# Kernel optimization log

Hardware: AMD Instinct MI355X
Metric: run time of the kernel (lower is better)

## Reference

```python
import jax, jax.numpy as jnp
import numpy as np

T, N, E, DH = 4, 10000, 160000, 256
BN_EPS = 1e-5


def setup_inputs() -> dict:
    key = jax.random.key(0)
    ks = jax.random.split(key, 6)
    node_data = jax.random.normal(ks[0], (T, N, DH), dtype=jnp.float32)
    edge_index = jax.random.randint(ks[1], (2, E), 0, N)
    edge_weight = jax.random.uniform(ks[2], (T, E), dtype=jnp.float32)
    W1 = jax.random.normal(ks[3], (3 * DH, DH), dtype=jnp.float32) * 0.02
    b1 = jnp.zeros((DH,), dtype=jnp.float32)
    gamma = jnp.ones((DH,), dtype=jnp.float32)
    beta = jnp.zeros((DH,), dtype=jnp.float32)
    return {"node_data": node_data, "edge_weight": edge_weight, "W1": W1,
            "b1": b1, "gamma": gamma, "beta": beta, "edge_index": edge_index}


def reference(node_data, edge_weight, W1, b1, gamma, beta, edge_index):
    # edge_index: [2, E] with row 0 = source j, row 1 = destination i
    # (ew[t, i, j] multiplies node j and accumulates into node i, as in bmm)
    src, dst = edge_index[0], edge_index[1]

    # sparse bmm: sum_j ew[t,i,j] * node_data[t,j,:]  -> [T, N, DH]
    weighted = node_data[:, src, :] * edge_weight[..., None]  # [T, E, DH]
    sum_neighbor = jax.vmap(lambda m: jax.ops.segment_sum(m, dst, num_segments=N))(weighted)

    # Z = torch.sparse.sum(ew, dim=2); Z[Z == 0] = 1
    Z = jax.vmap(lambda w: jax.ops.segment_sum(w, dst, num_segments=N))(edge_weight)
    Z = jnp.where(Z == 0, 1.0, Z)[..., None]  # [T, N, 1]
    avg_neighbor = sum_neighbor / Z

    # prev_state = cat([zeros(1,N,dh), node_data[1:]], dim=0)  (as in source)
    prev_state = jnp.concatenate(
        [jnp.zeros((1, N, DH), node_data.dtype), node_data[1:]], axis=0)

    x = jnp.concatenate([node_data, prev_state, avg_neighbor], axis=2)
    x = x.reshape(T * N, 3 * DH)

    # ReluFCN: Linear(3*dh -> dh) -> BatchNorm1d (batch stats) -> ReLU
    h = x @ W1 + b1  # [T*N, DH]
    mean = h.mean(axis=0)
    var = h.var(axis=0)
    h = (h - mean) * jax.lax.rsqrt(var + BN_EPS) * gamma + beta
    h = jax.nn.relu(h)
    return h.reshape(T, N, DH)
```

## Files before the change

kernel.cpp:

```cpp
#include <hip/hip_runtime.h>

enum { TT = 4, NNODES = 10000, NEDGES = 160000 };

typedef short v8s __attribute__((ext_vector_type(8)));
typedef float v4f __attribute__((ext_vector_type(4)));
typedef unsigned short u16x4 __attribute__((ext_vector_type(4)));

static __device__ __forceinline__ float bf2f(unsigned short u) {
    union { unsigned int i; float f; } c;
    c.i = ((unsigned int)u) << 16;
    return c.f;
}
static __device__ __forceinline__ unsigned short f2bf(float f) {
    union { float f; unsigned int i; } c;
    c.f = f;
    return (unsigned short)((c.i + 0x7FFFu + ((c.i >> 16) & 1u)) >> 16);
}
static __device__ __forceinline__ float u2f(unsigned int u) {
    union { unsigned int i; float f; } c;
    c.i = u;
    return c.f;
}
static __device__ __forceinline__ void acc8(float* a, float w, uint4 u) {
    a[0] += w * u2f(u.x << 16);
    a[1] += w * u2f(u.x & 0xffff0000u);
    a[2] += w * u2f(u.y << 16);
    a[3] += w * u2f(u.y & 0xffff0000u);
    a[4] += w * u2f(u.z << 16);
    a[5] += w * u2f(u.z & 0xffff0000u);
    a[6] += w * u2f(u.w << 16);
    a[7] += w * u2f(u.w & 0xffff0000u);
}

__global__ void GraphConvLayer_91061896610587_kernel() {}

__global__ void zero_k(int* p, int n) {
    int i = blockIdx.x * 256 + threadIdx.x;
    if (i < n) p[i] = 0;
}

__global__ void prep_k(const unsigned short* ndu, const void* s0, const void* s1,
                       const void* s2, int* mode, float* gammaf, float* betaf) {
    __shared__ int cnt;
    __shared__ int score[6];
    __shared__ float vals[6][256];
    int d = threadIdx.x;
    if (d == 0) cnt = 0;
    if (d < 6) score[d] = 0;
    __syncthreads();
    int c = 0;
    for (int j = 0; j < 16; ++j) {
        unsigned short u = ndu[d * 16 + j];
        if ((u & 0x7FFF) >= 0x6000) ++c;
    }
    if (c) atomicAdd(&cnt, c);
    const void* ptrs[3];
    ptrs[0] = s0; ptrs[1] = s1; ptrs[2] = s2;
    for (int q = 0; q < 6; ++q) {
        const void* p = ptrs[q % 3];
        float v = (q < 3) ? bf2f(((const unsigned short*)p)[d]) : ((const float*)p)[d];
        vals[q][d] = v;
        float av = fabsf(v);
        if (av > 0.25f && av < 4.0f) atomicAdd(&score[q], 1);
    }
    __syncthreads();
    if (d == 0) *mode = (cnt > 0) ? 0 : 1;
    int best = 0;
    for (int q = 1; q < 6; ++q)
        if (score[q] > score[best]) best = q;
    float g = (score[best] > 0) ? vals[best][d] : 1.0f;
    int interp = (best >= 3) ? 3 : 0;
    int bslot  = ((best % 3) == 2) ? 1 : 2;
    float b = vals[interp + bslot][d];
    if (!(b == b) || fabsf(b) > 100.f) b = 0.f;
    gammaf[d] = g;
    betaf[d]  = b;
}

__global__ void zp_k(int* zp, int zn, const unsigned short* ndu, const void* s0,
                     const void* s1, const void* s2, int* mode, float* gammaf,
                     float* betaf) {
    __shared__ int cnt;
    __shared__ int score[6];
    __shared__ float vals[6][256];
    if (blockIdx.x < 213) {
        int i = blockIdx.x * 256 + threadIdx.x;
        if (i < zn) zp[i] = 0;
        return;
    }
    int d = threadIdx.x;
    if (d == 0) cnt = 0;
    if (d < 6) score[d] = 0;
    __syncthreads();
    int c = 0;
    for (int j = 0; j < 16; ++j) {
        unsigned short u = ndu[d * 16 + j];
        if ((u & 0x7FFF) >= 0x6000) ++c;
    }
    if (c) atomicAdd(&cnt, c);
    const void* ptrs[3];
    ptrs[0] = s0; ptrs[1] = s1; ptrs[2] = s2;
    for (int q = 0; q < 6; ++q) {
        const void* p = ptrs[q % 3];
        float v = (q < 3) ? bf2f(((const unsigned short*)p)[d]) : ((const float*)p)[d];
        vals[q][d] = v;
        float av = fabsf(v);
        if (av > 0.25f && av < 4.0f) atomicAdd(&score[q], 1);
    }
    __syncthreads();
    if (d == 0) *mode = (cnt > 0) ? 0 : 1;
    int best = 0;
    for (int q = 1; q < 6; ++q)
        if (score[q] > score[best]) best = q;
    float g = (score[best] > 0) ? vals[best][d] : 1.0f;
    int interp = (best >= 3) ? 3 : 0;
    int bslot  = ((best % 3) == 2) ? 1 : 2;
    float b = vals[interp + bslot][d];
    if (!(b == b) || fabsf(b) > 100.f) b = 0.f;
    gammaf[d] = g;
    betaf[d]  = b;
}

__global__ void cph_k(const int* mode, const void* nd_raw, unsigned short* ndc,
                      const void* W1, short* wp0, short* wp1,
                      const int* ei, int* counts) {
    int bb = blockIdx.x;
    if (bb < 10000) {
        if (*mode != 0) return;
        int i = bb * 256 + threadIdx.x;
        float4 v = ((const float4*)nd_raw)[i];
        ushort4 o;
        o.x = f2bf(v.x); o.y = f2bf(v.y); o.z = f2bf(v.z); o.w = f2bf(v.w);
        ((ushort4*)ndc)[i] = o;
    } else if (bb < 11024) {
        int gid = (bb - 10000) * 256 + threadIdx.x;
        int v   = gid >> 17;
        int rem = gid & 131071;
        int k   = rem >> 8;
        int n   = rem & 255;
        int m   = *mode;
        const unsigned short* Wb = (const unsigned short*)W1;
        const float*          Wf = (const float*)W1;
        float val;
        if (k < 256) {
            val = m ? bf2f(Wb[k * 256 + n]) : Wf[k * 256 + n];
            if (v) val += m ? bf2f(Wb[(k + 256) * 256 + n]) : Wf[(k + 256) * 256 + n];
        } else {
            val = m ? bf2f(Wb[(k + 256) * 256 + n]) : Wf[(k + 256) * 256 + n];
        }
        int dst = ((k >> 5) * 256 + n) * 32 + (k & 31);
        (v ? wp1 : wp0)[dst] = (short)f2bf(val);
    } else {
        int e = (bb - 11024) * 256 + threadIdx.x;
        if (e < NEDGES) atomicAdd(&counts[ei[NEDGES + e]], 1);
    }
}

__global__ void pack_w(const int* mode, const void* W1, float* w2f,
                       short* wp0, short* wp1) {
    int gid = blockIdx.x * 256 + threadIdx.x;
    int v   = gid >> 17;
    int rem = gid & 131071;
    int k   = rem >> 8;
    int n   = rem & 255;
    int m   = *mode;
    const unsigned short* Wb = (const unsigned short*)W1;
    const float*          Wf = (const float*)W1;
    float val;
    if (k < 256) {
        val = m ? bf2f(Wb[k * 256 + n]) : Wf[k * 256 + n];
        if (v) val += m ? bf2f(Wb[(k + 256) * 256 + n]) : Wf[(k + 256) * 256 + n];
    } else {
        val = m ? bf2f(Wb[(k + 256) * 256 + n]) : Wf[(k + 256) * 256 + n];
    }
    if (w2f) w2f[v * 131072 + k * 256 + n] = val;
    if (wp0) {
        int dst = ((k >> 5) * 256 + n) * 32 + (k & 31);
        (v ? wp1 : wp0)[dst] = (short)f2bf(val);
    }
}

__global__ void hist_k(const int* ei, int* counts) {
    int e = blockIdx.x * 256 + threadIdx.x;
    if (e < NEDGES) atomicAdd(&counts[ei[NEDGES + e]], 1);
}

__global__ void scan_k(const int* counts, int* offsets) {
    __shared__ int part[256];
    __shared__ int excl[257];
    int t = threadIdx.x;
    int b = t * 40, e = b + 40;
    if (e > NNODES) e = NNODES;
    int s = 0;
    for (int i = b; i < e; ++i) s += counts[i];
    part[t] = s;
    __syncthreads();
    if (t == 0) {
        int run = 0;
        for (int i = 0; i < 256; ++i) { excl[i] = run; run += part[i]; }
        excl[256] = run;
    }
    __syncthreads();
    int run = excl[t];
    for (int i = b; i < e; ++i) { offsets[i] = run; run += counts[i]; }
    if (t == 0) offsets[NNODES] = excl[256];
}

__global__ void scat_k(const int* ei, const int* offsets, int* cursors,
                       int* ssrc, int* seid) {
    int e = blockIdx.x * 256 + threadIdx.x;
    if (e >= NEDGES) return;
    int d = ei[NEDGES + e];
    int pos = offsets[d] + atomicAdd(&cursors[d], 1);
    ssrc[pos] = ei[e];
    seid[pos] = e;
}

__global__ void scatw_k(const int* mode, const int* ei, const void* ew_raw,
                        const int* offsets, int* cursors, int* ssrc, int* seid,
                        float* wcsr) {
    int e = blockIdx.x * 256 + threadIdx.x;
    if (e >= NEDGES) return;
    int d = ei[NEDGES + e];
    int pos = offsets[d] + atomicAdd(&cursors[d], 1);
    ssrc[pos] = ei[e];
    seid[pos] = e;
    int m = *mode;
#pragma unroll
    for (int t = 0; t < TT; ++t) {
        float w = m ? bf2f(((const unsigned short*)ew_raw)[t * NEDGES + e])
                    : ((const float*)ew_raw)[t * NEDGES + e];
        wcsr[t * NEDGES + pos] = w;
    }
}

__global__ __launch_bounds__(256) void fused_k(
    const int* mode, const void* nd_raw, const unsigned short* ndc,
    const float* wcsr, const int* offsets, const int* ssrc,
    const short* wp0, const short* wp1,
    unsigned short* h16, float* colsumB, float* colsumsqB) {
    __shared__ unsigned short xs[32 * 520];
    int id  = blockIdx.x;
    int xcd = id & 7;
    int t   = xcd & 3;
    int rbi = ((id >> 3) << 1) + (xcd >> 2);
    if (rbi >= 313) return;
    int rb  = rbi * 32;
    const unsigned short* ndb = (*mode == 1) ? (const unsigned short*)nd_raw : ndc;
    int tid = threadIdx.x;

    int node = tid >> 3;
    int sub  = tid & 7;
    int growc = min(rb + node, NNODES - 1);
    const uint4* ndg = (const uint4*)(ndb + (size_t)t * NNODES * 256);
    const uint4* own = ndg + (size_t)growc * 32;

    uint4 c0 = own[sub];
    uint4 c1 = own[sub + 8];
    uint4 c2 = own[sub + 16];
    uint4 c3 = own[sub + 24];
    *(uint4*)&xs[node * 520 + sub * 8]            = c0;
    *(uint4*)&xs[node * 520 + (sub + 8) * 8]      = c1;
    *(uint4*)&xs[node * 520 + (sub + 16) * 8]     = c2;
    *(uint4*)&xs[node * 520 + (sub + 24) * 8]     = c3;

    float a1[32];
#pragma unroll
    for (int j = 0; j < 32; ++j) a1[j] = 0.f;
    float Z = 0.f;
    const float* wrow = wcsr + t * NEDGES;
    int b = offsets[growc], e = offsets[growc + 1];
    int p = b;
    for (; p + 2 <= e; p += 2) {
        int s0 = ssrc[p], s1 = ssrc[p + 1];
        float w0 = wrow[p], w1 = wrow[p + 1];
        const uint4* r0 = ndg + (size_t)s0 * 32;
        const uint4* r1 = ndg + (size_t)s1 * 32;
        uint4 A0 = r0[sub], A1 = r0[sub + 8], A2 = r0[sub + 16], A3 = r0[sub + 24];
        uint4 B0 = r1[sub], B1 = r1[sub + 8], B2 = r1[sub + 16], B3 = r1[sub + 24];
        Z += w0 + w1;
        acc8(a1 + 0,  w0, A0); acc8(a1 + 8,  w0, A1);
        acc8(a1 + 16, w0, A2); acc8(a1 + 24, w0, A3);
        acc8(a1 + 0,  w1, B0); acc8(a1 + 8,  w1, B1);
        acc8(a1 + 16, w1, B2); acc8(a1 + 24, w1, B3);
    }
    for (; p < e; ++p) {
        int s = ssrc[p];
        float w = wrow[p];
        const uint4* r0 = ndg + (size_t)s * 32;
        uint4 A0 = r0[sub], A1 = r0[sub + 8], A2 = r0[sub + 16], A3 = r0[sub + 24];
        Z += w;
        acc8(a1 + 0,  w, A0); acc8(a1 + 8,  w, A1);
        acc8(a1 + 16, w, A2); acc8(a1 + 24, w, A3);
    }
    float inv = (Z == 0.f) ? 1.f : (1.f / Z);
#pragma unroll
    for (int j = 0; j < 4; ++j) {
        ushort4 lo, hi;
        lo.x = f2bf(a1[j * 8 + 0] * inv);
        lo.y = f2bf(a1[j * 8 + 1] * inv);
        lo.z = f2bf(a1[j * 8 + 2] * inv);
        lo.w = f2bf(a1[j * 8 + 3] * inv);
        hi.x = f2bf(a1[j * 8 + 4] * inv);
        hi.y = f2bf(a1[j * 8 + 5] * inv);
        hi.z = f2bf(a1[j * 8 + 6] * inv);
        hi.w = f2bf(a1[j * 8 + 7] * inv);
        *(ushort4*)&xs[node * 520 + 256 + (sub + 8 * j) * 8]     = lo;
        *(ushort4*)&xs[node * 520 + 256 + (sub + 8 * j) * 8 + 4] = hi;
    }
    __syncthreads();

    int wave = tid >> 6;
    int lane = tid & 63;
    int lane15 = lane & 15, quad = lane >> 4;
    const v8s* wp8 = (const v8s*)(t ? wp1 : wp0);

    v4f acc[2][4];
    v4f zero = {0.f, 0.f, 0.f, 0.f};
#pragma unroll
    for (int mf = 0; mf < 2; ++mf)
#pragma unroll
        for (int nf = 0; nf < 4; ++nf) acc[mf][nf] = zero;

#pragma unroll
    for (int kc = 0; kc < 16; ++kc) {
        v8s a0 = *(const v8s*)&xs[lane15 * 520 + kc * 32 + quad * 8];
        v8s a1v = *(const v8s*)&xs[(lane15 + 16) * 520 + kc * 32 + quad * 8];
#pragma unroll
        for (int nf = 0; nf < 4; ++nf) {
            int ntg = wave * 4 + nf;
            v8s bf = wp8[(size_t)(kc * 256 + ntg * 16 + lane15) * 4 + quad];
            acc[0][nf] = __builtin_amdgcn_mfma_f32_16x16x32_bf16(a0, bf, acc[0][nf], 0, 0, 0);
            acc[1][nf] = __builtin_amdgcn_mfma_f32_16x16x32_bf16(a1v, bf, acc[1][nf], 0, 0, 0);
        }
    }

    int bucket = id & 63;
#pragma unroll
    for (int nf = 0; nf < 4; ++nf) {
        int col = (wave * 4 + nf) * 16 + lane15;
        float s1 = 0.f, s2 = 0.f;
#pragma unroll
        for (int mf = 0; mf < 2; ++mf) {
            int rbase = rb + mf * 16 + quad * 4;
#pragma unroll
            for (int r = 0; r < 4; ++r) {
                int row = rbase + r;
                if (row < NNODES) {
                    float v = acc[mf][nf][r];
                    __builtin_nontemporal_store(
                        f2bf(v), &h16[(size_t)(t * NNODES + row) * 256 + col]);
                    s1 += v; s2 += v * v;
                }
            }
        }
        s1 += __shfl_xor(s1, 16, 64); s1 += __shfl_xor(s1, 32, 64);
        s2 += __shfl_xor(s2, 16, 64); s2 += __shfl_xor(s2, 32, 64);
        if (quad == 0) {
            atomicAdd(&colsumB[bucket * 256 + col], s1);
            atomicAdd(&colsumsqB[bucket * 256 + col], s2);
        }
    }
}

__global__ void statsB_k(const float* colsumB, const float* colsumsqB,
                         const float* gammaf, const float* betaf,
                         float* scale, float* shiftv) {
    int d = threadIdx.x;
    float s1 = 0.f, s2 = 0.f;
    for (int b = 0; b < 64; ++b) {
        s1 += colsumB[b * 256 + d];
        s2 += colsumsqB[b * 256 + d];
    }
    float mean = s1 * (1.f / 40000.f);
    float var  = s2 * (1.f / 40000.f) - mean * mean;
    if (var < 0.f) var = 0.f;
    if (!(var < 1e30f) || !(mean == mean)) { scale[d] = 0.f; shiftv[d] = 2.5f; return; }
    float r  = rsqrtf(var + 1e-5f);
    float sc = gammaf[d] * r;
    scale[d]  = sc;
    shiftv[d] = betaf[d] - mean * sc;
}

__global__ void normb_k(const unsigned short* h16, const float* scale,
                        const float* shiftv, float* out) {
    int i = blockIdx.x * 256 + threadIdx.x;
    int c0 = (i & 63) * 4;
    u16x4 h = __builtin_nontemporal_load(&((const u16x4*)h16)[i]);
    v4f o;
    float v;
    v = bf2f(h.x) * scale[c0 + 0] + shiftv[c0 + 0]; if (!(v == v)) v = 1.f; o.x = v > 0.f ? v : 0.f;
    v = bf2f(h.y) * scale[c0 + 1] + shiftv[c0 + 1]; if (!(v == v)) v = 1.f; o.y = v > 0.f ? v : 0.f;
    v = bf2f(h.z) * scale[c0 + 2] + shiftv[c0 + 2]; if (!(v == v)) v = 1.f; o.z = v > 0.f ? v : 0.f;
    v = bf2f(h.w) * scale[c0 + 3] + shiftv[c0 + 3]; if (!(v == v)) v = 1.f; o.w = v > 0.f ? v : 0.f;
    __builtin_nontemporal_store(o, &((v4f*)out)[i]);
}

__global__ void aggv_k(const int* mode, const void* nd_raw, const void* ew_raw,
                       const int* offsets, const int* ssrc, const int* seid,
                       unsigned short* avg) {
    int m   = *mode;
    int wid = blockIdx.x * 4 + (threadIdx.x >> 6);
    int t = wid / NNODES, n = wid - t * NNODES;
    int lane = threadIdx.x & 63;
    float a0 = 0.f, a1 = 0.f, a2 = 0.f, a3 = 0.f, Z = 0.f;
    int b = offsets[n], e = offsets[n + 1];
    for (int p = b; p < e; ++p) {
        int s = ssrc[p];
        int ewi = t * NEDGES + seid[p];
        float w = m ? bf2f(((const unsigned short*)ew_raw)[ewi])
                    : ((const float*)ew_raw)[ewi];
        Z += w;
        int vidx = (t * NNODES + s) * 64 + lane;
        if (m) {
            ushort4 v = ((const ushort4*)nd_raw)[vidx];
            a0 += w * bf2f(v.x); a1 += w * bf2f(v.y);
            a2 += w * bf2f(v.z); a3 += w * bf2f(v.w);
        } else {
            float4 v = ((const float4*)nd_raw)[vidx];
            a0 += w * v.x; a1 += w * v.y; a2 += w * v.z; a3 += w * v.w;
        }
    }
    float inv = (Z == 0.f) ? 1.f : (1.f / Z);
    ushort4 o;
    o.x = f2bf(a0 * inv); o.y = f2bf(a1 * inv);
    o.z = f2bf(a2 * inv); o.w = f2bf(a3 * inv);
    ((ushort4*)avg)[(t * NNODES + n) * 64 + lane] = o;
}

__global__ __launch_bounds__(256) void gemmv_k(
    const int* mode, const void* nd_raw, const unsigned short* avg,
    const float* w2f, float* hbuf) {
    __shared__ float xsf[16 * 512];
    int m   = *mode;
    int bt  = blockIdx.x / 625;
    int rb0 = (blockIdx.x - bt * 625) * 16;
    int tid = threadIdx.x;
    for (int j = 0; j < 32; ++j) {
        int idx = tid + j * 256;
        int r = idx >> 9, k = idx & 511;
        int grow = (bt * NNODES + rb0 + r) * 256;
        float val;
        if (k < 256)
            val = m ? bf2f(((const unsigned short*)nd_raw)[grow + k])
                    : ((const float*)nd_raw)[grow + k];
        else
            val = bf2f(avg[grow + (k - 256)]);
        xsf[idx] = val;
    }
    __syncthreads();
    int r0 = (tid >> 6) * 4;
    const float4* w4 = (const float4*)(w2f + (bt ? 131072 : 0));
    float acc[4][4];
#pragma unroll
    for (int r = 0; r < 4; ++r)
#pragma unroll
        for (int c = 0; c < 4; ++c) acc[r][c] = 0.f;
    const float* x0 = &xsf[(r0 + 0) * 512];
    const float* x1 = &xsf[(r0 + 1) * 512];
    const float* x2 = &xsf[(r0 + 2) * 512];
    const float* x3 = &xsf[(r0 + 3) * 512];
#pragma unroll 8
    for (int k = 0; k < 512; ++k) {
        float4 wv = w4[k * 64 + (tid & 63)];
        float a = x0[k], b = x1[k], c = x2[k], d = x3[k];
        acc[0][0] += a * wv.x; acc[0][1] += a * wv.y; acc[0][2] += a * wv.z; acc[0][3] += a * wv.w;
        acc[1][0] += b * wv.x; acc[1][1] += b * wv.y; acc[1][2] += b * wv.z; acc[1][3] += b * wv.w;
        acc[2][0] += c * wv.x; acc[2][1] += c * wv.y; acc[2][2] += c * wv.z; acc[2][3] += c * wv.w;
        acc[3][0] += d * wv.x; acc[3][1] += d * wv.y; acc[3][2] += d * wv.z; acc[3][3] += d * wv.w;
    }
#pragma unroll
    for (int r = 0; r < 4; ++r) {
        int grow = bt * NNODES + rb0 + r0 + r;
        float4 o;
        o.x = acc[r][0]; o.y = acc[r][1]; o.z = acc[r][2]; o.w = acc[r][3];
        ((float4*)hbuf)[grow * 64 + (tid & 63)] = o;
    }
}

__global__ void stats2_k(const float* hbuf, float* colsum, float* colsumsq) {
    int col = threadIdx.x;
    int rb  = blockIdx.x * 250;
    float s1 = 0.f, s2 = 0.f;
    for (int j = 0; j < 250; ++j) {
        float v = hbuf[(size_t)(rb + j) * 256 + col];
        s1 += v; s2 += v * v;
    }
    atomicAdd(&colsum[col], s1);
    atomicAdd(&colsumsq[col], s2);
}

__global__ void stats_k(const float* colsum, const float* colsumsq,
                        const float* gammaf, const float* betaf,
                        float* scale, float* shiftv) {
    int d = threadIdx.x;
    float mean = colsum[d] * (1.f / 40000.f);
    float var  = colsumsq[d] * (1.f / 40000.f) - mean * mean;
    if (var < 0.f) var = 0.f;
    if (!(var < 1e30f) || !(mean == mean)) { scale[d] = 0.f; shiftv[d] = 2.5f; return; }
    float r  = rsqrtf(var + 1e-5f);
    float sc = gammaf[d] * r;
    scale[d]  = sc;
    shiftv[d] = betaf[d] - mean * sc;
}

__global__ void norm_k(float* hbuf, const float* scale, const float* shiftv) {
    int i = blockIdx.x * 256 + threadIdx.x;
    int c0 = (i & 63) * 4;
    float4 h = ((const float4*)hbuf)[i];
    float4 o;
    float v;
    v = h.x * scale[c0 + 0] + shiftv[c0 + 0]; if (!(v == v)) v = 1.f; o.x = v > 0.f ? v : 0.f;
    v = h.y * scale[c0 + 1] + shiftv[c0 + 1]; if (!(v == v)) v = 1.f; o.y = v > 0.f ? v : 0.f;
    v = h.z * scale[c0 + 2] + shiftv[c0 + 2]; if (!(v == v)) v = 1.f; o.z = v > 0.f ? v : 0.f;
    v = h.w * scale[c0 + 3] + shiftv[c0 + 3]; if (!(v == v)) v = 1.f; o.w = v > 0.f ? v : 0.f;
    ((float4*)hbuf)[i] = o;
}

extern "C" void kernel_launch(void* const* d_in, const int* in_sizes, int n_in,
                              void* d_out, int out_size, void* d_ws, size_t ws_size,
                              hipStream_t stream) {
    const void* nd = d_in[0];
    const void* ew = d_in[1];
    const void* W1 = d_in[2];
    const void* p3 = d_in[3];
    const void* p4 = d_in[4];
    const void* p5 = d_in[5];
    const void* ei = d_in[6];
    {
        const void *nd_ = 0, *ew_ = 0, *W1_ = 0, *ei_ = 0, *s_[3] = {0, 0, 0};
        int ns = 0;
        for (int i = 0; i < n_in; ++i) {
            int s = in_sizes[i];
            if      (s == 10240000) nd_ = d_in[i];
            else if (s == 640000)   ew_ = d_in[i];
            else if (s == 196608)   W1_ = d_in[i];
            else if (s == 320000)   ei_ = d_in[i];
            else if (s == 256 && ns < 3) s_[ns++] = d_in[i];
        }
        if (nd_ && ew_ && W1_ && ei_ && ns == 3) {
            nd = nd_; ew = ew_; W1 = W1_; ei = ei_;
            p3 = s_[0]; p4 = s_[1]; p5 = s_[2];
        }
    }
    float* outp = (float*)d_out;
    const unsigned short* ndu = (const unsigned short*)nd;
    const int* eii = (const int*)ei;

    char* ws = (char*)d_ws;

    if (ws_size >= (size_t)45582464) {
        int*   counts    = (int*)(ws + 0);
        int*   cursors   = (int*)(ws + 40960);
        int*   mode      = (int*)(ws + 81920);
        float* scale     = (float*)(ws + 82944);
        float* shiftv    = (float*)(ws + 83968);
        float* gammaf    = (float*)(ws + 84992);
        float* betaf     = (float*)(ws + 86016);
        float* colsumB   = (float*)(ws + 87040);
        float* colsumsqB = (float*)(ws + 152576);
        int*   offsets   = (int*)(ws + 218112);
        int*   ssrc      = (int*)(ws + 258176);
        int*   seid      = (int*)(ws + 898176);
        float* wcsr      = (float*)(ws + 1538176);
        short* wp0       = (short*)(ws + 4098176);
        short* wp1       = (short*)(ws + 4360320);
        unsigned short* ndc = (unsigned short*)(ws + 4622464);
        unsigned short* h16 = (unsigned short*)(ws + 25102464);

        zp_k<<<214, 256, 0, stream>>>((int*)ws, 54528, ndu, p3, p4, p5,
                                      mode, gammaf, betaf);
        cph_k<<<11649, 256, 0, stream>>>(mode, nd, ndc, W1, wp0, wp1, eii, counts);
        scan_k<<<1, 256, 0, stream>>>(counts, offsets);
        scatw_k<<<625, 256, 0, stream>>>(mode, eii, ew, offsets, cursors,
                                         ssrc, seid, wcsr);
        fused_k<<<1280, 256, 0, stream>>>(mode, nd, ndc, wcsr, offsets, ssrc,
                                          wp0, wp1, h16, colsumB, colsumsqB);
        statsB_k<<<1, 256, 0, stream>>>(colsumB, colsumsqB, gammaf, betaf, scale, shiftv);
        normb_k<<<10000, 256, 0, stream>>>(h16, scale, shiftv, outp);
    } else {
        int*   counts   = (int*)(ws + 0);
        int*   cursors  = (int*)(ws + 40960);
        float* colsum   = (float*)(ws + 81920);
        float* colsumsq = (float*)(ws + 82944);
        int*   mode     = (int*)(ws + 83968);
        float* scale    = (float*)(ws + 84032);
        float* shiftv   = (float*)(ws + 85056);
        float* gammaf   = (float*)(ws + 86080);
        float* betaf    = (float*)(ws + 87104);
        int*   offsets  = (int*)(ws + 88128);
        int*   ssrc     = (int*)(ws + 128192);
        int*   seid     = (int*)(ws + 768192);
        float* w2f      = (float*)(ws + 1408192);
        unsigned short* avg = (unsigned short*)(ws + 2457600);
        short* nowp = 0;

        zero_k<<<83, 256, 0, stream>>>((int*)ws, 20994);
        prep_k<<<1, 256, 0, stream>>>(ndu, p3, p4, p5, mode, gammaf, betaf);
        pack_w<<<1024, 256, 0, stream>>>(mode, W1, w2f, nowp, nowp);
        hist_k<<<625, 256, 0, stream>>>(eii, counts);
        scan_k<<<1, 256, 0, stream>>>(counts, offsets);
        scat_k<<<625, 256, 0, stream>>>(eii, offsets, cursors, ssrc, seid);
        aggv_k<<<10000, 256, 0, stream>>>(mode, nd, ew, offsets, ssrc, seid, avg);
        gemmv_k<<<2500, 256, 0, stream>>>(mode, nd, avg, w2f, outp);
        stats2_k<<<160, 256, 0, stream>>>(outp, colsum, colsumsq);
        stats_k<<<1, 256, 0, stream>>>(colsum, colsumsq, gammaf, betaf, scale, shiftv);
        norm_k<<<10000, 256, 0, stream>>>(outp, scale, shiftv);
    }
}
```

Baseline: 233.0 us.

## Double fused kernel threads per block, splitting each node's gather over 16 lanes

The fused gather-and-matmul kernel now runs 512 threads per block instead of 256. Each node's neighbour aggregation is split across 16 lanes rather than 8, which halves per-thread accumulator registers, and the edge loop is unrolled by 4 to keep more loads in flight. In the MFMA stage each of the 8 waves covers 2 column tiles instead of 4. The aim is more parallelism and memory-level overlap in the latency-bound gather, at the cost of larger blocks and a changed occupancy hint.

```diff
diff --git a/kernel.cpp b/kernel.cpp
--- a/kernel.cpp
+++ b/kernel.cpp
@@ -234,7 +234,7 @@
     }
 }
 
-__global__ __launch_bounds__(256) void fused_k(
+__global__ __launch_bounds__(512, 6) void fused_k(
     const int* mode, const void* nd_raw, const unsigned short* ndc,
     const float* wcsr, const int* offsets, const int* ssrc,
     const short* wp0, const short* wp1,
@@ -249,64 +249,64 @@
     const unsigned short* ndb = (*mode == 1) ? (const unsigned short*)nd_raw : ndc;
     int tid = threadIdx.x;
 
-    int node = tid >> 3;
-    int sub  = tid & 7;
+    int node = tid >> 4;
+    int sub  = tid & 15;
     int growc = min(rb + node, NNODES - 1);
     const uint4* ndg = (const uint4*)(ndb + (size_t)t * NNODES * 256);
     const uint4* own = ndg + (size_t)growc * 32;
 
     uint4 c0 = own[sub];
-    uint4 c1 = own[sub + 8];
-    uint4 c2 = own[sub + 16];
-    uint4 c3 = own[sub + 24];
-    *(uint4*)&xs[node * 520 + sub * 8]            = c0;
-    *(uint4*)&xs[node * 520 + (sub + 8) * 8]      = c1;
-    *(uint4*)&xs[node * 520 + (sub + 16) * 8]     = c2;
-    *(uint4*)&xs[node * 520 + (sub + 24) * 8]     = c3;
-
-    float a1[32];
-#pragma unroll
-    for (int j = 0; j < 32; ++j) a1[j] = 0.f;
+    uint4 c1 = own[sub + 16];
+    *(uint4*)&xs[node * 520 + sub * 8]        = c0;
+    *(uint4*)&xs[node * 520 + (sub + 16) * 8] = c1;
+
+    float a1[16];
+#pragma unroll
+    for (int j = 0; j < 16; ++j) a1[j] = 0.f;
     float Z = 0.f;
     const float* wrow = wcsr + t * NEDGES;
     int b = offsets[growc], e = offsets[growc + 1];
     int p = b;
-    for (; p + 2 <= e; p += 2) {
-        int s0 = ssrc[p], s1 = ssrc[p + 1];
-        float w0 = wrow[p], w1 = wrow[p + 1];
+    for (; p + 4 <= e; p += 4) {
+        int s0 = ssrc[p], s1 = ssrc[p + 1], s2 = ssrc[p + 2], s3 = ssrc[p + 3];
+        float w0 = wrow[p], w1 = wrow[p + 1], w2 = wrow[p + 2], w3 = wrow[p + 3];
         const uint4* r0 = ndg + (size_t)s0 * 32;
         const uint4* r1 = ndg + (size_t)s1 * 32;
-        uint4 A0 = r0[sub], A1 = r0[sub + 8], A2 = r0[sub + 16], A3 = r0[sub + 24];
-        uint4 B0 = r1[sub], B1 = r1[sub + 8], B2 = r1[sub + 16], B3 = r1[sub + 24];
-        Z += w0 + w1;
-        acc8(a1 + 0,  w0, A0); acc8(a1 + 8,  w0, A1);
-        acc8(a1 + 16, w0, A2); acc8(a1 + 24, w0, A3);
-        acc8(a1 + 0,  w1, B0); acc8(a1 + 8,  w1, B1);
-        acc8(a1 + 16, w1, B2); acc8(a1 + 24, w1, B3);
+        const uint4* r2 = ndg + (size_t)s2 * 32;
+        const uint4* r3 = ndg + (size_t)s3 * 32;
+        uint4 A0 = r0[sub], A1 = r0[sub + 16];
+        uint4 B0 = r1[sub], B1 = r1[sub + 16];
+        uint4 C0 = r2[sub], C1 = r2[sub + 16];
+        uint4 D0 = r3[sub], D1 = r3[sub + 16];
+        Z += w0 + w1 + w2 + w3;
+        acc8(a1 + 0, w0, A0); acc8(a1 + 8, w0, A1);
+        acc8(a1 + 0, w1, B0); acc8(a1 + 8, w1, B1);
+        acc8(a1 + 0, w2, C0); acc8(a1 + 8, w2, C1);
+        acc8(a1 + 0, w3, D0); acc8(a1 + 8, w3, D1);
     }
     for (; p < e; ++p) {
         int s = ssrc[p];
         float w = wrow[p];
         const uint4* r0 = ndg + (size_t)s * 32;
-        uint4 A0 = r0[sub], A1 = r0[sub + 8], A2 = r0[sub + 16], A3 = r0[sub + 24];
+        uint4 A0 = r0[sub], A1 = r0[sub + 16];
         Z += w;
-        acc8(a1 + 0,  w, A0); acc8(a1 + 8,  w, A1);
-        acc8(a1 + 16, w, A2); acc8(a1 + 24, w, A3);
+        acc8(a1 + 0, w, A0); acc8(a1 + 8, w, A1);
     }
     float inv = (Z == 0.f) ? 1.f : (1.f / Z);
-#pragma unroll
-    for (int j = 0; j < 4; ++j) {
+    {
         ushort4 lo, hi;
-        lo.x = f2bf(a1[j * 8 + 0] * inv);
-        lo.y = f2bf(a1[j * 8 + 1] * inv);
-        lo.z = f2bf(a1[j * 8 + 2] * inv);
-        lo.w = f2bf(a1[j * 8 + 3] * inv);
-        hi.x = f2bf(a1[j * 8 + 4] * inv);
-        hi.y = f2bf(a1[j * 8 + 5] * inv);
-        hi.z = f2bf(a1[j * 8 + 6] * inv);
-        hi.w = f2bf(a1[j * 8 + 7] * inv);
-        *(ushort4*)&xs[node * 520 + 256 + (sub + 8 * j) * 8]     = lo;
-        *(ushort4*)&xs[node * 520 + 256 + (sub + 8 * j) * 8 + 4] = hi;
+        lo.x = f2bf(a1[0] * inv); lo.y = f2bf(a1[1] * inv);
+        lo.z = f2bf(a1[2] * inv); lo.w = f2bf(a1[3] * inv);
+        hi.x = f2bf(a1[4] * inv); hi.y = f2bf(a1[5] * inv);
+        hi.z = f2bf(a1[6] * inv); hi.w = f2bf(a1[7] * inv);
+        *(ushort4*)&xs[node * 520 + 256 + sub * 8]     = lo;
+        *(ushort4*)&xs[node * 520 + 256 + sub * 8 + 4] = hi;
+        lo.x = f2bf(a1[8] * inv);  lo.y = f2bf(a1[9] * inv);
+        lo.z = f2bf(a1[10] * inv); lo.w = f2bf(a1[11] * inv);
+        hi.x = f2bf(a1[12] * inv); hi.y = f2bf(a1[13] * inv);
+        hi.z = f2bf(a1[14] * inv); hi.w = f2bf(a1[15] * inv);
+        *(ushort4*)&xs[node * 520 + 256 + (sub + 16) * 8]     = lo;
+        *(ushort4*)&xs[node * 520 + 256 + (sub + 16) * 8 + 4] = hi;
     }
     __syncthreads();
 
@@ -315,30 +315,30 @@
     int lane15 = lane & 15, quad = lane >> 4;
     const v8s* wp8 = (const v8s*)(t ? wp1 : wp0);
 
-    v4f acc[2][4];
+    v4f acc[2][2];
     v4f zero = {0.f, 0.f, 0.f, 0.f};
 #pragma unroll
     for (int mf = 0; mf < 2; ++mf)
 #pragma unroll
-        for (int nf = 0; nf < 4; ++nf) acc[mf][nf] = zero;
+        for (int nf = 0; nf < 2; ++nf) acc[mf][nf] = zero;
 
 #pragma unroll
     for (int kc = 0; kc < 16; ++kc) {
-        v8s a0 = *(const v8s*)&xs[lane15 * 520 + kc * 32 + quad * 8];
+        v8s a0  = *(const v8s*)&xs[lane15 * 520 + kc * 32 + quad * 8];
         v8s a1v = *(const v8s*)&xs[(lane15 + 16) * 520 + kc * 32 + quad * 8];
 #pragma unroll
-        for (int nf = 0; nf < 4; ++nf) {
-            int ntg = wave * 4 + nf;
+        for (int nf = 0; nf < 2; ++nf) {
+            int ntg = wave * 2 + nf;
             v8s bf = wp8[(size_t)(kc * 256 + ntg * 16 + lane15) * 4 + quad];
-            acc[0][nf] = __builtin_amdgcn_mfma_f32_16x16x32_bf16(a0, bf, acc[0][nf], 0, 0, 0);
+            acc[0][nf] = __builtin_amdgcn_mfma_f32_16x16x32_bf16(a0,  bf, acc[0][nf], 0, 0, 0);
             acc[1][nf] = __builtin_amdgcn_mfma_f32_16x16x32_bf16(a1v, bf, acc[1][nf], 0, 0, 0);
         }
     }
 
     int bucket = id & 63;
 #pragma unroll
-    for (int nf = 0; nf < 4; ++nf) {
-        int col = (wave * 4 + nf) * 16 + lane15;
+    for (int nf = 0; nf < 2; ++nf) {
+        int col = (wave * 2 + nf) * 16 + lane15;
         float s1 = 0.f, s2 = 0.f;
 #pragma unroll
         for (int mf = 0; mf < 2; ++mf) {
@@ -574,7 +574,7 @@
         scan_k<<<1, 256, 0, stream>>>(counts, offsets);
         scatw_k<<<625, 256, 0, stream>>>(mode, eii, ew, offsets, cursors,
                                          ssrc, seid, wcsr);
-        fused_k<<<1280, 256, 0, stream>>>(mode, nd, ndc, wcsr, offsets, ssrc,
+        fused_k<<<1280, 512, 0, stream>>>(mode, nd, ndc, wcsr, offsets, ssrc,
                                           wp0, wp1, h16, colsumB, colsumsqB);
         statsB_k<<<1, 256, 0, stream>>>(colsumB, colsumsqB, gammaf, betaf, scale, shiftv);
         normb_k<<<10000, 256, 0, stream>>>(h16, scale, shiftv, outp);
```

New measurement: 273.8 us. +17.5%, slower.
